# Performance work log

Measured on AMD Instinct MI355X. Metric: run time of the kernel, lower is better.

The kernel has to match this reference:

```python
import jax, jax.numpy as jnp
import numpy as np

N = 50000   # nodes (= batch_size = num_e)
D = 256     # d_dim = n_hidden
E = 320000  # edges (first half 'in' direction, second half 'out'/inverse)
R = 400     # relation types (incl. inverses)


def setup_inputs() -> dict:
    key = jax.random.key(0)
    ks = jax.random.split(key, 12)
    s = 0.05  # weight scale so tanh stays in linear-ish range
    w = lambda k, shp: jax.random.normal(k, shp, jnp.float32) * s
    return {
        "emb": jax.random.normal(ks[0], (N, D), jnp.float32),
        "edge_index": jax.random.randint(ks[1], (2, E), 0, N),
        "edge_type": jax.random.randint(ks[2], (E,), 0, R),
        "rel1": w(ks[3], (R, D)),
        "W_in1": w(ks[4], (D, D)),
        "W_out1": w(ks[5], (D, D)),
        "W_loop1": w(ks[6], (D, D)),
        "b1": jnp.zeros((D,), jnp.float32),
        "rel2": w(ks[7], (R, D)),
        "W_in2": w(ks[8], (D, D)),
        "W_out2": w(ks[9], (D, D)),
        "W_loop2": w(ks[10], (D, D)),
        "b2": jnp.zeros((D,), jnp.float32),
        "res": jnp.array([0.1], jnp.float32),
        "mu_w": w(ks[11], (D, D)),
        "mu_b": jnp.zeros((D,), jnp.float32),
        "num_nodes": N,
    }


def _mgcn_conv(x, edge_index, edge_type, rel, W_in, W_out, W_loop, b, n):
    """Relational conv: gather -> compose with relation emb -> direction-split
    linear transform -> degree-normalized scatter-add -> self-loop -> tanh."""
    src, dst = edge_index[0], edge_index[1]
    e = edge_index.shape[1]
    half = e // 2
    m = x[src] * rel[edge_type]                                   # [E, D] compose ('mult')
    m = jnp.concatenate([m[:half] @ W_in, m[half:] @ W_out], 0)    # direction-specific transform
    deg = jax.ops.segment_sum(jnp.ones((e,), x.dtype), dst, num_segments=n)
    norm = 1.0 / jnp.maximum(deg, 1.0)                             # 1/in-degree
    agg = jax.ops.segment_sum(m * norm[dst][:, None], dst, num_segments=n)
    return jnp.tanh(agg + x @ W_loop + b)


def reference(emb, edge_index, edge_type,
              rel1, W_in1, W_out1, W_loop1, b1,
              rel2, W_in2, W_out2, W_loop2, b2,
              res, mu_w, mu_b, num_nodes):
    # forward_base with p.res=True, core_layer=2, dropout in eval mode (identity)
    h = emb + res * _mgcn_conv(emb, edge_index, edge_type, rel1, W_in1, W_out1, W_loop1, b1, num_nodes)
    h = h + res * _mgcn_conv(h, edge_index, edge_type, rel2, W_in2, W_out2, W_loop2, b2, num_nodes)
    # drift head f(t, y) = mu(forward_base(y))
    return h @ mu_w + mu_b
```

## Files before the change

### kernel.cpp

```cpp
#include <hip/hip_runtime.h>
#include <hip/hip_bf16.h>
#include <cstdint>
#include <cstddef>


typedef short bf16x8 __attribute__((ext_vector_type(8)));
typedef float f32x4  __attribute__((ext_vector_type(4)));

__device__ __forceinline__ float b2f(unsigned short u) {
    union { unsigned u32; float f; } c; c.u32 = ((unsigned)u) << 16; return c.f;
}
__device__ __forceinline__ unsigned short f2b(float f) {
    union { float f; unsigned u; } c; c.f = f;
    unsigned r = c.u + 0x7FFFu + ((c.u >> 16) & 1u);
    return (unsigned short)(r >> 16);
}
__device__ __forceinline__ float ftanh(float x) {
    float e = __expf(2.0f * x);
    return 1.0f - __fdividef(2.0f, e + 1.0f);
}


__global__ void k_hist(const int* __restrict__ dst, int* __restrict__ cnt, int E) {
    int i = blockIdx.x * blockDim.x + threadIdx.x;
    if (i < E) atomicAdd(&cnt[dst[i]], 1);
}

__global__ void k_norm(const int* __restrict__ cnt, float* __restrict__ norm, int N) {
    int i = blockIdx.x * blockDim.x + threadIdx.x;
    if (i < N) norm[i] = 1.0f / fmaxf((float)cnt[i], 1.0f);
}

__global__ void k_scan1(const int* __restrict__ cnt, int* __restrict__ part,
                        int* __restrict__ bsum, int N) {
    __shared__ int s[256];
    int i = blockIdx.x * 256 + threadIdx.x;
    int v = (i < N) ? cnt[i] : 0;
    s[threadIdx.x] = v; __syncthreads();
    #pragma unroll
    for (int o = 1; o < 256; o <<= 1) {
        int t = (threadIdx.x >= o) ? s[threadIdx.x - o] : 0;
        __syncthreads();
        s[threadIdx.x] += t;
        __syncthreads();
    }
    if (i < N) part[i] = s[threadIdx.x] - v;
    if (threadIdx.x == 255) bsum[blockIdx.x] = s[255];
}

__global__ void k_scan2(int* __restrict__ bsum, int nb) {
    __shared__ int s[256];
    int v = (threadIdx.x < nb) ? bsum[threadIdx.x] : 0;
    s[threadIdx.x] = v; __syncthreads();
    #pragma unroll
    for (int o = 1; o < 256; o <<= 1) {
        int t = (threadIdx.x >= o) ? s[threadIdx.x - o] : 0;
        __syncthreads();
        s[threadIdx.x] += t;
        __syncthreads();
    }
    if (threadIdx.x < nb) bsum[threadIdx.x] = s[threadIdx.x] - v;
}

__global__ void k_scan3(const int* __restrict__ part, const int* __restrict__ bsum,
                        int* __restrict__ rowptr, int* __restrict__ cursor, int N, int E) {
    int i = blockIdx.x * 256 + threadIdx.x;
    if (i < N) {
        int r = part[i] + bsum[blockIdx.x];
        rowptr[i] = r; cursor[i] = r;
    }
    if (i == 0) rowptr[N] = E;
}

__global__ void k_scatter(const int* __restrict__ src, const int* __restrict__ dst,
                          const int* __restrict__ et, int* __restrict__ cursor,
                          unsigned* __restrict__ erec, int E, int halfE) {
    int e = blockIdx.x * blockDim.x + threadIdx.x;
    if (e < E) {
        int d = dst[e];
        int pos = atomicAdd(&cursor[d], 1);
        unsigned rec = (unsigned)src[e] | ((unsigned)et[e] << 16)
                     | ((e >= halfE) ? 0x80000000u : 0u);
        erec[pos] = rec;
    }
}


__global__ void k_cvt3(const float* __restrict__ s0, unsigned short* __restrict__ d0, long n0,
                       const float* __restrict__ s1, unsigned short* __restrict__ d1, long n1,
                       const float* __restrict__ s2, unsigned short* __restrict__ d2, long n2) {
    long i = (long)blockIdx.x * blockDim.x + threadIdx.x;
    const float* s; unsigned short* d; long j = i;
    if (j < n0) { s = s0; d = d0; }
    else {
        j -= n0;
        if (j < n1) { s = s1; d = d1; }
        else { j -= n1; if (j >= n2) return; s = s2; d = d2; }
    }
    float4 v = ((const float4*)s)[j];
    ushort4 o;
    o.x = f2b(v.x); o.y = f2b(v.y); o.z = f2b(v.z); o.w = f2b(v.w);
    ((ushort4*)d)[j] = o;
}

__global__ void k_wfrag7(const float* __restrict__ w0, const float* __restrict__ w1,
                         const float* __restrict__ w2, const float* __restrict__ w3,
                         const float* __restrict__ w4, const float* __restrict__ w5,
                         const float* __restrict__ w6, unsigned short* __restrict__ out) {
    int o = blockIdx.x * 256 + threadIdx.x;
    int mi = o >> 16;
    int r  = o & 65535;
    const float* W = (mi == 0) ? w0 : (mi == 1) ? w1 : (mi == 2) ? w2 :
                     (mi == 3) ? w3 : (mi == 4) ? w4 : (mi == 5) ? w5 : w6;
    int j  = r & 7;
    int l  = (r >> 3) & 63;
    int nn = (r >> 9) & 15;
    int kg = r >> 13;
    int k = kg * 32 + (l >> 4) * 8 + j;
    int n = nn * 16 + (l & 15);
    out[o] = f2b(W[k * 256 + n]);
}


__global__ __launch_bounds__(256)
void k_agg(const unsigned short* __restrict__ xb, const unsigned short* __restrict__ relb,
           const int* __restrict__ rowptr, const unsigned* __restrict__ erec,
           const float* __restrict__ norm,
           unsigned short* __restrict__ sIn, unsigned short* __restrict__ sOut,
           int N, int D)
{
    const int w = threadIdx.x >> 6, l = threadIdx.x & 63;
    const int v = blockIdx.x * 4 + w;
    if (v >= N) return;
    const int rs = rowptr[v], re = rowptr[v + 1];
    const float nm = norm[v];

    float ai0 = 0, ai1 = 0, ai2 = 0, ai3 = 0;
    float ao0 = 0, ao1 = 0, ao2 = 0, ao3 = 0;

    unsigned c0 = (rs     < re) ? erec[rs]     : 0u;
    unsigned c1 = (rs + 1 < re) ? erec[rs + 1] : 0u;
    unsigned c2 = (rs + 2 < re) ? erec[rs + 2] : 0u;
    unsigned c3 = (rs + 3 < re) ? erec[rs + 3] : 0u;
    int i = rs;
    while (i + 4 <= re) {
        unsigned m0 = (i + 4 < re) ? erec[i + 4] : 0u;
        unsigned m1 = (i + 5 < re) ? erec[i + 5] : 0u;
        unsigned m2 = (i + 6 < re) ? erec[i + 6] : 0u;
        unsigned m3 = (i + 7 < re) ? erec[i + 7] : 0u;
        ushort4 x0 = *(const ushort4*)(xb   + (size_t)(c0 & 0xffff) * D + l * 4);
        ushort4 r0 = *(const ushort4*)(relb + (size_t)((c0 >> 16) & 0x7fff) * D + l * 4);
        ushort4 x1 = *(const ushort4*)(xb   + (size_t)(c1 & 0xffff) * D + l * 4);
        ushort4 r1 = *(const ushort4*)(relb + (size_t)((c1 >> 16) & 0x7fff) * D + l * 4);
        ushort4 x2 = *(const ushort4*)(xb   + (size_t)(c2 & 0xffff) * D + l * 4);
        ushort4 r2 = *(const ushort4*)(relb + (size_t)((c2 >> 16) & 0x7fff) * D + l * 4);
        ushort4 x3 = *(const ushort4*)(xb   + (size_t)(c3 & 0xffff) * D + l * 4);
        ushort4 r3 = *(const ushort4*)(relb + (size_t)((c3 >> 16) & 0x7fff) * D + l * 4);
        float p0, p1, p2, p3;
        p0 = b2f(x0.x)*b2f(r0.x); p1 = b2f(x0.y)*b2f(r0.y);
        p2 = b2f(x0.z)*b2f(r0.z); p3 = b2f(x0.w)*b2f(r0.w);
        if (c0 >> 31) { ao0 += p0; ao1 += p1; ao2 += p2; ao3 += p3; }
        else          { ai0 += p0; ai1 += p1; ai2 += p2; ai3 += p3; }
        p0 = b2f(x1.x)*b2f(r1.x); p1 = b2f(x1.y)*b2f(r1.y);
        p2 = b2f(x1.z)*b2f(r1.z); p3 = b2f(x1.w)*b2f(r1.w);
        if (c1 >> 31) { ao0 += p0; ao1 += p1; ao2 += p2; ao3 += p3; }
        else          { ai0 += p0; ai1 += p1; ai2 += p2; ai3 += p3; }
        p0 = b2f(x2.x)*b2f(r2.x); p1 = b2f(x2.y)*b2f(r2.y);
        p2 = b2f(x2.z)*b2f(r2.z); p3 = b2f(x2.w)*b2f(r2.w);
        if (c2 >> 31) { ao0 += p0; ao1 += p1; ao2 += p2; ao3 += p3; }
        else          { ai0 += p0; ai1 += p1; ai2 += p2; ai3 += p3; }
        p0 = b2f(x3.x)*b2f(r3.x); p1 = b2f(x3.y)*b2f(r3.y);
        p2 = b2f(x3.z)*b2f(r3.z); p3 = b2f(x3.w)*b2f(r3.w);
        if (c3 >> 31) { ao0 += p0; ao1 += p1; ao2 += p2; ao3 += p3; }
        else          { ai0 += p0; ai1 += p1; ai2 += p2; ai3 += p3; }
        c0 = m0; c1 = m1; c2 = m2; c3 = m3; i += 4;
    }
    #pragma unroll
    for (int j = 0; j < 3; ++j) {
        if (i + j < re) {
            unsigned cur = (j == 0) ? c0 : (j == 1) ? c1 : c2;
            ushort4 x0 = *(const ushort4*)(xb   + (size_t)(cur & 0xffff) * D + l * 4);
            ushort4 r0 = *(const ushort4*)(relb + (size_t)((cur >> 16) & 0x7fff) * D + l * 4);
            float p0 = b2f(x0.x)*b2f(r0.x), p1 = b2f(x0.y)*b2f(r0.y);
            float p2 = b2f(x0.z)*b2f(r0.z), p3 = b2f(x0.w)*b2f(r0.w);
            if (cur >> 31) { ao0 += p0; ao1 += p1; ao2 += p2; ao3 += p3; }
            else           { ai0 += p0; ai1 += p1; ai2 += p2; ai3 += p3; }
        }
    }

    ushort4 oi, oo;
    oi.x = f2b(ai0 * nm); oi.y = f2b(ai1 * nm); oi.z = f2b(ai2 * nm); oi.w = f2b(ai3 * nm);
    oo.x = f2b(ao0 * nm); oo.y = f2b(ao1 * nm); oo.z = f2b(ao2 * nm); oo.w = f2b(ao3 * nm);
    *(ushort4*)(sIn  + (size_t)v * D + l * 4) = oi;
    *(ushort4*)(sOut + (size_t)v * D + l * 4) = oo;
}


__global__ __launch_bounds__(256, 2)
void k_gemmW(const unsigned short* __restrict__ a0,
             const unsigned short* __restrict__ a1,
             const unsigned short* __restrict__ a2,
             const unsigned short* __restrict__ Wf,
             const float* __restrict__ bias,
             const float* __restrict__ resPtr,
             unsigned short* __restrict__ outB,
             int N, int D)
{
    __shared__ unsigned short lds[4][2][4096];

    const int t = threadIdx.x;
    const int rBase = blockIdx.x * 64;
    const int w  = t >> 6;
    const int l  = t & 63;
    const int lr = l & 15;
    const int lq = l >> 4;

    size_t gRow[8];
    #pragma unroll
    for (int j = 0; j < 8; ++j)
        gRow[j] = (size_t)min(rBase + j * 8 + (l >> 3), N - 1) * 256 + (l & 7) * 8;
    const int woBase = (l >> 3) * 64 + (((l & 7) ^ (l >> 3)) * 8);

    f32x4 acc[4][4] = {};
    uint4 Rg[8];

    #pragma unroll
    for (int j = 0; j < 8; ++j)
        Rg[j] = *(const uint4*)(a0 + gRow[j]);
    #pragma unroll
    for (int j = 0; j < 8; ++j)
        *(uint4*)(&lds[w][0][woBase + j * 512]) = Rg[j];
    #pragma unroll
    for (int j = 0; j < 8; ++j)
        Rg[j] = *(const uint4*)(a0 + gRow[j] + 64);

    #pragma unroll
    for (int s = 0; s < 12; ++s) {
        const unsigned short* __restrict__ At = lds[w][s & 1];
        const int p = s >> 2, cb = s & 3;
        const unsigned short* __restrict__ Wp = Wf + (size_t)p * 65536;

        if (s + 1 < 12) {
            unsigned short* An = &lds[w][(s + 1) & 1][0];
            #pragma unroll
            for (int j = 0; j < 8; ++j)
                *(uint4*)(&An[woBase + j * 512]) = Rg[j];
        }
        if (s + 2 < 12) {
            const int p2 = (s + 2) >> 2, cb2 = (s + 2) & 3;
            const unsigned short* ap = (p2 == 0) ? a0 : ((p2 == 1) ? a1 : a2);
            #pragma unroll
            for (int j = 0; j < 8; ++j)
                Rg[j] = *(const uint4*)(ap + gRow[j] + cb2 * 64);
        }
        (void)cb;

        #pragma unroll
        for (int kk = 0; kk < 2; ++kk) {
            const int kg = cb * 2 + kk;
            bf16x8 a_[4], b_[4];
            #pragma unroll
            for (int m = 0; m < 4; ++m) {
                int rm = 16 * m + lr;
                int ch = (kk * 4 + lq) ^ (rm & 7);
                a_[m] = *(const bf16x8*)(&At[rm * 64 + ch * 8]);
            }
            #pragma unroll
            for (int n = 0; n < 4; ++n)
                b_[n] = *(const bf16x8*)(Wp + (((kg * 16 + (w * 4 + n)) * 64 + l) * 8));
            #pragma unroll
            for (int m = 0; m < 4; ++m) {
                #pragma unroll
                for (int n = 0; n < 4; ++n)
                    acc[m][n] = __builtin_amdgcn_mfma_f32_16x16x32_bf16(a_[m], b_[n], acc[m][n], 0, 0, 0);
            }
        }
    }

    const int rb4 = lq * 4;
    const float resv = resPtr[0];
    unsigned short* C = (unsigned short*)lds;
    __syncthreads();
    #pragma unroll
    for (int half = 0; half < 2; ++half) {
        if (half) __syncthreads();
        if ((w >> 1) == half) {
            #pragma unroll
            for (int m = 0; m < 4; ++m) {
                #pragma unroll
                for (int i = 0; i < 4; ++i) {
                    int r6 = 16 * m + rb4 + i;
                    #pragma unroll
                    for (int n = 0; n < 4; ++n) {
                        int cH = (w & 1) * 64 + lr + 16 * n;
                        float v = acc[m][n][i] + bias[half * 128 + cH];
                        C[r6 * 128 + cH] = f2b(resv * ftanh(v));
                    }
                }
            }
        }
        __syncthreads();
        #pragma unroll
        for (int ii = 0; ii < 4; ++ii) {
            int g   = ii * 256 + t;
            int r   = g >> 4;
            int cc  = g & 15;
            int row = rBase + r;
            if (row < N) {
                bf16x8 sv = *(const bf16x8*)(&C[r * 128 + cc * 8]);
                const unsigned short* ar = a0 + (size_t)row * D + half * 128 + cc * 8;
                uint4 av = *(const uint4*)ar;
                unsigned aw[4] = { av.x, av.y, av.z, av.w };
                unsigned ow[4];
                #pragma unroll
                for (int p = 0; p < 4; ++p) {
                    float h0 = b2f((unsigned short)(aw[p] & 0xffff)) + b2f((unsigned short)sv[2 * p]);
                    float h1 = b2f((unsigned short)(aw[p] >> 16))    + b2f((unsigned short)sv[2 * p + 1]);
                    ow[p] = (unsigned)f2b(h0) | ((unsigned)f2b(h1) << 16);
                }
                *(uint4*)(outB + (size_t)row * D + half * 128 + cc * 8) =
                    make_uint4(ow[0], ow[1], ow[2], ow[3]);
            }
        }
    }
}


#define GIT(S, AtC, AtN, Rw0, Rw1, Rl0, Rl1, Bc, Bn)                            \
  do {                                                                          \
    if ((S) + 1 < 12) {                                                         \
      *(uint4*)(&AtN[wo0]) = Rw0;                                               \
      *(uint4*)(&AtN[wo1]) = Rw1;                                               \
    }                                                                           \
    if ((S) + 1 < 12) {                                                         \
      const int pn_ = ((S) + 1) >> 2, cbn_ = ((S) + 1) & 3;                     \
      const unsigned short* __restrict__ Wn_ = Wf + (size_t)pn_ * 65536;        \
      _Pragma("unroll")                                                         \
      for (int kk_ = 0; kk_ < 2; ++kk_) {                                       \
        _Pragma("unroll")                                                       \
        for (int n_ = 0; n_ < 4; ++n_) {                                        \
          Bn[kk_ * 4 + n_] = *(const bf16x8*)(Wn_ +                             \
              ((((cbn_ * 2 + kk_) * 16 + (w * 4 + n_)) * 64 + l) * 8));         \
        }                                                                       \
      }                                                                         \
    }                                                                           \
    {                                                                           \
      const int cb_ = (S) & 3;                                                  \
      _Pragma("unroll")                                                         \
      for (int kk_ = 0; kk_ < 2; ++kk_) {                                       \
        (void)cb_;                                                              \
        bf16x8 a_[4];                                                           \
        _Pragma("unroll")                                                       \
        for (int m_ = 0; m_ < 4; ++m_) {                                        \
          int rm_ = 16 * m_ + lr;                                               \
          int ch_ = (kk_ * 4 + lq) ^ (rm_ & 7);                                 \
          a_[m_] = *(const bf16x8*)(&AtC[rm_ * 64 + ch_ * 8]);                  \
        }                                                                       \
        _Pragma("unroll")                                                       \
        for (int m_ = 0; m_ < 4; ++m_) {                                        \
          _Pragma("unroll")                                                     \
          for (int n_ = 0; n_ < 4; ++n_) {                                      \
            acc[m_][n_] = __builtin_amdgcn_mfma_f32_16x16x32_bf16(a_[m_], Bc[kk_ * 4 + n_], acc[m_][n_], 0, 0, 0); \
          }                                                                     \
        }                                                                       \
      }                                                                         \
    }                                                                           \
    if ((S) + 3 < 12) {                                                         \
      const int p3_ = ((S) + 3) >> 2, cb3_ = ((S) + 3) & 3;                     \
      const unsigned short* ap_ = (p3_ == 0) ? a0 : ((p3_ == 1) ? a1 : a2);     \
      Rl0 = *(const uint4*)(ap_ + g0 + cb3_ * 64);                              \
      Rl1 = *(const uint4*)(ap_ + g1 + cb3_ * 64);                              \
    }                                                                           \
    asm volatile("s_waitcnt lgkmcnt(0)" ::: "memory");                          \
    __builtin_amdgcn_sched_barrier(0);                                          \
    __builtin_amdgcn_s_barrier();                                               \
    __builtin_amdgcn_sched_barrier(0);                                          \
  } while (0)

template <bool HEAD>
__global__ __launch_bounds__(256, 2)
void k_gemm(const unsigned short* __restrict__ a0,
            const unsigned short* __restrict__ a1,
            const unsigned short* __restrict__ a2,
            const unsigned short* __restrict__ Wf,
            const float* __restrict__ bias,
            const float* __restrict__ resPtr,
            const unsigned short* __restrict__ WfMu,
            const float* __restrict__ mub,
            float* __restrict__ outF,
            unsigned short* __restrict__ outB,
            int N, int D)
{
    __shared__ unsigned short lds[HEAD ? 16384 : 8192];
    unsigned short* At0 = lds;
    unsigned short* At1 = lds + 4096;

    const int t = threadIdx.x;
    const int rBase = blockIdx.x * 64;

    const int w  = t >> 6;
    const int l  = t & 63;
    const int lr = l & 15;
    const int lq = l >> 4;

    const int rS0 = t >> 3;
    const int rS1 = rS0 + 32;
    const int cS  = t & 7;
    const int wo0 = rS0 * 64 + ((cS ^ (rS0 & 7)) * 8);
    const int wo1 = rS1 * 64 + ((cS ^ (rS1 & 7)) * 8);
    const size_t g0 = (size_t)min(rBase + rS0, N - 1) * D + cS * 8;
    const size_t g1 = (size_t)min(rBase + rS1, N - 1) * D + cS * 8;

    f32x4 acc[4][4] = {};
    uint4 Ra0, Ra1, Rb0, Rb1, Rc0, Rc1;
    bf16x8 B0[8], B1[8];

    Ra0 = *(const uint4*)(a0 + g0);
    Ra1 = *(const uint4*)(a0 + g1);
    Rb0 = *(const uint4*)(a0 + g0 + 64);
    Rb1 = *(const uint4*)(a0 + g1 + 64);
    Rc0 = *(const uint4*)(a0 + g0 + 128);
    Rc1 = *(const uint4*)(a0 + g1 + 128);
    #pragma unroll
    for (int kk = 0; kk < 2; ++kk) {
        #pragma unroll
        for (int n = 0; n < 4; ++n)
            B0[kk * 4 + n] = *(const bf16x8*)(Wf + (((kk * 16 + (w * 4 + n)) * 64 + l) * 8));
    }
    *(uint4*)(&At0[wo0]) = Ra0;
    *(uint4*)(&At0[wo1]) = Ra1;
    asm volatile("s_waitcnt lgkmcnt(0)" ::: "memory");
    __builtin_amdgcn_sched_barrier(0);
    __builtin_amdgcn_s_barrier();
    __builtin_amdgcn_sched_barrier(0);

    GIT(0,  At0, At1, Rb0, Rb1, Ra0, Ra1, B0, B1);
    GIT(1,  At1, At0, Rc0, Rc1, Rb0, Rb1, B1, B0);
    GIT(2,  At0, At1, Ra0, Ra1, Rc0, Rc1, B0, B1);
    GIT(3,  At1, At0, Rb0, Rb1, Ra0, Ra1, B1, B0);
    GIT(4,  At0, At1, Rc0, Rc1, Rb0, Rb1, B0, B1);
    GIT(5,  At1, At0, Ra0, Ra1, Rc0, Rc1, B1, B0);
    GIT(6,  At0, At1, Rb0, Rb1, Ra0, Ra1, B0, B1);
    GIT(7,  At1, At0, Rc0, Rc1, Rb0, Rb1, B1, B0);
    GIT(8,  At0, At1, Ra0, Ra1, Rc0, Rc1, B0, B1);
    GIT(9,  At1, At0, Rb0, Rb1, Ra0, Ra1, B1, B0);
    GIT(10, At0, At1, Rc0, Rc1, Rb0, Rb1, B0, B1);
    GIT(11, At1, At0, Ra0, Ra1, Rc0, Rc1, B1, B0);

    const int rb4 = lq * 4;
    const float resv = resPtr[0];

    if (!HEAD) {
        unsigned short* C = lds;
        #pragma unroll
        for (int half = 0; half < 2; ++half) {
            if ((w >> 1) == half) {
                #pragma unroll
                for (int m = 0; m < 4; ++m) {
                    #pragma unroll
                    for (int i = 0; i < 4; ++i) {
                        int r6 = 16 * m + rb4 + i;
                        #pragma unroll
                        for (int n = 0; n < 4; ++n) {
                            int cH = (w & 1) * 64 + lr + 16 * n;
                            float v = acc[m][n][i] + bias[half * 128 + cH];
                            C[r6 * 128 + cH] = f2b(resv * ftanh(v));
                        }
                    }
                }
            }
            __syncthreads();
            #pragma unroll
            for (int ii = 0; ii < 4; ++ii) {
                int g   = ii * 256 + t;
                int r   = g >> 4;
                int cc  = g & 15;
                int row = rBase + r;
                if (row < N) {
                    bf16x8 sv = *(const bf16x8*)(&C[r * 128 + cc * 8]);
                    const unsigned short* ar = a0 + (size_t)row * D + half * 128 + cc * 8;
                    uint4 av = *(const uint4*)ar;
                    unsigned aw[4] = { av.x, av.y, av.z, av.w };
                    unsigned ow[4];
                    #pragma unroll
                    for (int p = 0; p < 4; ++p) {
                        float h0 = b2f((unsigned short)(aw[p] & 0xffff)) + b2f((unsigned short)sv[2 * p]);
                        float h1 = b2f((unsigned short)(aw[p] >> 16))    + b2f((unsigned short)sv[2 * p + 1]);
                        ow[p] = (unsigned)f2b(h0) | ((unsigned)f2b(h1) << 16);
                    }
                    *(uint4*)(outB + (size_t)row * D + half * 128 + cc * 8) =
                        make_uint4(ow[0], ow[1], ow[2], ow[3]);
                }
            }
            __syncthreads();
        }
    } else {
        #pragma unroll
        for (int m = 0; m < 4; ++m) {
            #pragma unroll
            for (int i = 0; i < 4; ++i) {
                int row = rBase + 16 * m + rb4 + i;
                if (row < N) {
                    size_t base = (size_t)row * D + w * 64 + lr;
                    int r6 = 16 * m + rb4 + i;
                    #pragma unroll
                    for (int n = 0; n < 4; ++n) {
                        int   c = w * 64 + lr + 16 * n;
                        float v = acc[m][n][i] + bias[c];
                        float h = b2f(a0[base + 16 * n]) + resv * ftanh(v);
                        lds[r6 * 256 + (c ^ ((r6 & 7) << 3))] = f2b(h);
                    }
                }
            }
        }
        __syncthreads();
        #pragma unroll
        for (int m = 0; m < 4; ++m) {
            #pragma unroll
            for (int n = 0; n < 4; ++n)
                acc[m][n] = (f32x4){0.f, 0.f, 0.f, 0.f};
        }

        #pragma unroll
        for (int s2 = 0; s2 < 4; ++s2) {
            #pragma unroll
            for (int kk = 0; kk < 2; ++kk) {
                const int kg = s2 * 2 + kk;
                bf16x8 a_[4], b_[4];
                #pragma unroll
                for (int m = 0; m < 4; ++m) {
                    int rm = 16 * m + lr;
                    int ch = (s2 * 8 + kk * 4 + lq) ^ (rm & 7);
                    a_[m] = *(const bf16x8*)(&lds[rm * 256 + ch * 8]);
                }
                #pragma unroll
                for (int n = 0; n < 4; ++n)
                    b_[n] = *(const bf16x8*)(WfMu + (((kg * 16 + (w * 4 + n)) * 64 + l) * 8));
                #pragma unroll
                for (int m = 0; m < 4; ++m) {
                    #pragma unroll
                    for (int n = 0; n < 4; ++n)
                        acc[m][n] = __builtin_amdgcn_mfma_f32_16x16x32_bf16(a_[m], b_[n], acc[m][n], 0, 0, 0);
                }
            }
        }

        __syncthreads();
        float* Cf = (float*)lds;
        #pragma unroll
        for (int half = 0; half < 2; ++half) {
            if ((w >> 1) == half) {
                #pragma unroll
                for (int m = 0; m < 4; ++m) {
                    #pragma unroll
                    for (int i = 0; i < 4; ++i) {
                        int r6 = 16 * m + rb4 + i;
                        #pragma unroll
                        for (int n = 0; n < 4; ++n) {
                            int cH = (w & 1) * 64 + lr + 16 * n;
                            Cf[r6 * 128 + cH] = acc[m][n][i] + mub[half * 128 + cH];
                        }
                    }
                }
            }
            __syncthreads();
            #pragma unroll
            for (int ii = 0; ii < 8; ++ii) {
                int g   = ii * 256 + t;
                int r   = g >> 5;
                int cc  = g & 31;
                int row = rBase + r;
                if (row < N) {
                    *(float4*)(outF + (size_t)row * D + half * 128 + cc * 4) =
                        *(const float4*)(&Cf[r * 128 + cc * 4]);
                }
            }
            __syncthreads();
        }
    }
}


extern "C" void kernel_launch(void* const* d_in, const int* in_sizes, int n_in,
                              void* d_out, int out_size, void* d_ws, size_t ws_size,
                              hipStream_t stream)
{
    const float* emb  = (const float*)d_in[0];
    const int*   ei   = (const int*)  d_in[1];
    const int*   et   = (const int*)  d_in[2];
    const float* rel1 = (const float*)d_in[3];
    const float* Wi1  = (const float*)d_in[4];
    const float* Wo1  = (const float*)d_in[5];
    const float* Wl1  = (const float*)d_in[6];
    const float* b1   = (const float*)d_in[7];
    const float* rel2 = (const float*)d_in[8];
    const float* Wi2  = (const float*)d_in[9];
    const float* Wo2  = (const float*)d_in[10];
    const float* Wl2  = (const float*)d_in[11];
    const float* b2   = (const float*)d_in[12];
    const float* res  = (const float*)d_in[13];
    const float* muw  = (const float*)d_in[14];
    const float* mub  = (const float*)d_in[15];

    const int D = in_sizes[7];
    const int N = in_sizes[0] / D;
    const int E = in_sizes[2];
    const int R = in_sizes[3] / D;
    const int halfE = E / 2;
    const int* srcA = ei;
    const int* dstA = ei + E;
    const size_t DD = (size_t)D * D;

    char* ws = (char*)d_ws;
    size_t off = 0;
    auto alloc = [&](size_t bytes) -> char* {
        char* p = ws + off; off += (bytes + 255) & ~(size_t)255; return p;
    };
    const int nb1 = (N + 255) / 256;

    float*          norm   = (float*)          alloc((size_t)N * 4);
    int*            cnt    = (int*)            alloc((size_t)N * 4);
    int*            rowptr = (int*)            alloc((size_t)(N + 1) * 4);
    int*            cursor = (int*)            alloc((size_t)N * 4);
    int*            part   = (int*)            alloc((size_t)N * 4);
    int*            bsum   = (int*)            alloc(1024);
    unsigned*       erec   = (unsigned*)       alloc((size_t)E * 4);
    unsigned short* xb     = (unsigned short*) alloc((size_t)N * D * 2);
    unsigned short* h1b    = (unsigned short*) alloc((size_t)N * D * 2);
    unsigned short* sIn    = (unsigned short*) alloc((size_t)N * D * 2);
    unsigned short* sOut   = (unsigned short*) alloc((size_t)N * D * 2);
    unsigned short* r1b    = (unsigned short*) alloc((size_t)R * D * 2);
    unsigned short* r2b    = (unsigned short*) alloc((size_t)R * D * 2);
    unsigned short* fAll   = (unsigned short*) alloc(7 * DD * 2);
    if (off > ws_size) return;

    unsigned short* fW1 = fAll;
    unsigned short* fW2 = fAll + 3 * DD;
    unsigned short* fMu = fAll + 6 * DD;

    hipMemsetAsync(cnt, 0, (size_t)N * 4, stream);
    k_hist   <<<(E + 255) / 256, 256, 0, stream>>>(dstA, cnt, E);
    k_norm   <<<nb1, 256, 0, stream>>>(cnt, norm, N);
    k_scan1  <<<nb1, 256, 0, stream>>>(cnt, part, bsum, N);
    k_scan2  <<<1,   256, 0, stream>>>(bsum, nb1);
    k_scan3  <<<nb1, 256, 0, stream>>>(part, bsum, rowptr, cursor, N, E);
    k_scatter<<<(E + 255) / 256, 256, 0, stream>>>(srcA, dstA, et, cursor, erec, E, halfE);

    long nd4 = (long)N * D / 4, rd4 = (long)R * D / 4;
    long tot4 = nd4 + 2 * rd4;
    k_cvt3<<<(int)((tot4 + 255) / 256), 256, 0, stream>>>(
        emb, xb, nd4, rel1, r1b, rd4, rel2, r2b, rd4);
    k_wfrag7<<<(int)(7 * DD / 256), 256, 0, stream>>>(
        Wl1, Wi1, Wo1, Wl2, Wi2, Wo2, muw, fAll);

    const int AB = (N + 3) / 4;
    const int NB = (N + 63) / 64;

    k_agg<<<AB, 256, 0, stream>>>(xb, r1b, rowptr, erec, norm, sIn, sOut, N, D);
    k_gemmW<<<NB, 256, 0, stream>>>(xb, sIn, sOut, fW1, b1, res, h1b, N, D);

    k_agg<<<AB, 256, 0, stream>>>(h1b, r2b, rowptr, erec, norm, sIn, sOut, N, D);
    k_gemm<true><<<NB, 256, 0, stream>>>(h1b, sIn, sOut, fW2, b2, res,
                                         fMu, mub, (float*)d_out, nullptr, N, D);
}
```

Measured before the change: 239.3 us.

## Use half-wave edge split in layer-1 aggregation and 512-thread shared-tile GEMM

Adds k_agg2, in which each half of a wavefront handles alternate edges with 16-byte loads covering all 256 columns, and the two halves' partial sums are combined with a cross-half shuffle. It also replaces the layer-1 GEMM with a 512-thread kernel where all eight waves share one 64-row A tile in LDS, with triple-register prefetch and block barriers between steps. The goals are more memory-level parallelism in the gather and less per-wave LDS use with higher occupancy in the GEMM. The cost is extra barriers and a shuffle reduction, and only layer 1 uses the new kernels.

```diff
diff --git a/kernel.cpp b/kernel.cpp
--- a/kernel.cpp
+++ b/kernel.cpp
@@ -119,6 +119,95 @@
     int k = kg * 32 + (l >> 4) * 8 + j;
     int n = nn * 16 + (l & 15);
     out[o] = f2b(W[k * 256 + n]);
+}
+
+
+__global__ __launch_bounds__(256)
+void k_agg2(const unsigned short* __restrict__ xb, const unsigned short* __restrict__ relb,
+            const int* __restrict__ rowptr, const unsigned* __restrict__ erec,
+            const float* __restrict__ norm,
+            unsigned short* __restrict__ sIn, unsigned short* __restrict__ sOut,
+            int N, int D)
+{
+    const int w = threadIdx.x >> 6, l = threadIdx.x & 63;
+    const int v = blockIdx.x * 4 + w;
+    if (v >= N) return;
+    const int rs = rowptr[v], re = rowptr[v + 1];
+    const float nm = norm[v];
+    const int h  = l >> 5;
+    const int sl = l & 31;
+
+    float ai[8] = {}, ao[8] = {};
+
+    #pragma unroll 1
+    for (int i = rs; i < re; i += 4) {
+        const int e0 = i + h, e1 = i + 2 + h;
+        const unsigned c0 = (e0 < re) ? erec[e0] : 0u;
+        const unsigned c1 = (e1 < re) ? erec[e1] : 0u;
+        uint4 x0 = make_uint4(0,0,0,0), r0 = make_uint4(0,0,0,0);
+        uint4 x1 = make_uint4(0,0,0,0), r1 = make_uint4(0,0,0,0);
+        if (e0 < re) {
+            x0 = *(const uint4*)(xb   + (size_t)(c0 & 0xffff) * 256 + sl * 8);
+            r0 = *(const uint4*)(relb + (size_t)((c0 >> 16) & 0x7fff) * 256 + sl * 8);
+        }
+        if (e1 < re) {
+            x1 = *(const uint4*)(xb   + (size_t)(c1 & 0xffff) * 256 + sl * 8);
+            r1 = *(const uint4*)(relb + (size_t)((c1 >> 16) & 0x7fff) * 256 + sl * 8);
+        }
+        {
+            unsigned xs[4] = { x0.x, x0.y, x0.z, x0.w };
+            unsigned rv[4] = { r0.x, r0.y, r0.z, r0.w };
+            if (c0 >> 31) {
+                #pragma unroll
+                for (int p = 0; p < 4; ++p) {
+                    ao[2*p]   += b2f((unsigned short)(xs[p] & 0xffff)) * b2f((unsigned short)(rv[p] & 0xffff));
+                    ao[2*p+1] += b2f((unsigned short)(xs[p] >> 16))    * b2f((unsigned short)(rv[p] >> 16));
+                }
+            } else {
+                #pragma unroll
+                for (int p = 0; p < 4; ++p) {
+                    ai[2*p]   += b2f((unsigned short)(xs[p] & 0xffff)) * b2f((unsigned short)(rv[p] & 0xffff));
+                    ai[2*p+1] += b2f((unsigned short)(xs[p] >> 16))    * b2f((unsigned short)(rv[p] >> 16));
+                }
+            }
+        }
+        {
+            unsigned xs[4] = { x1.x, x1.y, x1.z, x1.w };
+            unsigned rv[4] = { r1.x, r1.y, r1.z, r1.w };
+            if (c1 >> 31) {
+                #pragma unroll
+                for (int p = 0; p < 4; ++p) {
+                    ao[2*p]   += b2f((unsigned short)(xs[p] & 0xffff)) * b2f((unsigned short)(rv[p] & 0xffff));
+                    ao[2*p+1] += b2f((unsigned short)(xs[p] >> 16))    * b2f((unsigned short)(rv[p] >> 16));
+                }
+            } else {
+                #pragma unroll
+                for (int p = 0; p < 4; ++p) {
+                    ai[2*p]   += b2f((unsigned short)(xs[p] & 0xffff)) * b2f((unsigned short)(rv[p] & 0xffff));
+                    ai[2*p+1] += b2f((unsigned short)(xs[p] >> 16))    * b2f((unsigned short)(rv[p] >> 16));
+                }
+            }
+        }
+    }
+
+    #pragma unroll
+    for (int j = 0; j < 8; ++j) {
+        ai[j] += __shfl_xor(ai[j], 32, 64);
+        ao[j] += __shfl_xor(ao[j], 32, 64);
+    }
+
+    unsigned ow[4];
+    if (h == 0) {
+        #pragma unroll
+        for (int p = 0; p < 4; ++p)
+            ow[p] = (unsigned)f2b(ai[2*p] * nm) | ((unsigned)f2b(ai[2*p+1] * nm) << 16);
+        *(uint4*)(sIn + (size_t)v * 256 + sl * 8) = make_uint4(ow[0], ow[1], ow[2], ow[3]);
+    } else {
+        #pragma unroll
+        for (int p = 0; p < 4; ++p)
+            ow[p] = (unsigned)f2b(ao[2*p] * nm) | ((unsigned)f2b(ao[2*p+1] * nm) << 16);
+        *(uint4*)(sOut + (size_t)v * 256 + sl * 8) = make_uint4(ow[0], ow[1], ow[2], ow[3]);
+    }
 }
 
 
@@ -196,103 +285,115 @@
 }
 
 
-__global__ __launch_bounds__(256, 2)
-void k_gemmW(const unsigned short* __restrict__ a0,
-             const unsigned short* __restrict__ a1,
-             const unsigned short* __restrict__ a2,
-             const unsigned short* __restrict__ Wf,
-             const float* __restrict__ bias,
-             const float* __restrict__ resPtr,
-             unsigned short* __restrict__ outB,
-             int N, int D)
+#define GIT512(S, AtC, AtN, Rw, Rl)                                            \
+  do {                                                                         \
+    if ((S) + 1 < 12) {                                                        \
+      *(uint4*)(&AtN[wo]) = Rw;                                                \
+    }                                                                          \
+    {                                                                          \
+      const int p_ = (S) >> 2, cb_ = (S) & 3;                                  \
+      const unsigned short* __restrict__ Wp_ = Wf + (size_t)p_ * 65536;        \
+      _Pragma("unroll")                                                        \
+      for (int kk_ = 0; kk_ < 2; ++kk_) {                                      \
+        const int kg_ = cb_ * 2 + kk_;                                         \
+        bf16x8 a_[2], b_[4];                                                   \
+        _Pragma("unroll")                                                      \
+        for (int m_ = 0; m_ < 2; ++m_) {                                       \
+          int rm_ = 32 * wm + 16 * m_ + lr;                                    \
+          int ch_ = (kk_ * 4 + lq) ^ (rm_ & 7);                                \
+          a_[m_] = *(const bf16x8*)(&AtC[rm_ * 64 + ch_ * 8]);                 \
+        }                                                                      \
+        _Pragma("unroll")                                                      \
+        for (int n_ = 0; n_ < 4; ++n_) {                                       \
+          b_[n_] = *(const bf16x8*)(Wp_ + (((kg_ * 16 + (wcol * 4 + n_)) * 64 + l) * 8)); \
+        }                                                                      \
+        _Pragma("unroll")                                                      \
+        for (int m_ = 0; m_ < 2; ++m_) {                                       \
+          _Pragma("unroll")                                                    \
+          for (int n_ = 0; n_ < 4; ++n_) {                                     \
+            acc[m_][n_] = __builtin_amdgcn_mfma_f32_16x16x32_bf16(a_[m_], b_[n_], acc[m_][n_], 0, 0, 0); \
+          }                                                                    \
+        }                                                                      \
+      }                                                                        \
+    }                                                                          \
+    if ((S) + 3 < 12) {                                                        \
+      const int p3_ = ((S) + 3) >> 2, cb3_ = ((S) + 3) & 3;                    \
+      const unsigned short* ap_ = (p3_ == 0) ? a0 : ((p3_ == 1) ? a1 : a2);    \
+      Rl = *(const uint4*)(ap_ + g + cb3_ * 64);                               \
+    }                                                                          \
+    asm volatile("s_waitcnt lgkmcnt(0)" ::: "memory");                         \
+    __builtin_amdgcn_sched_barrier(0);                                         \
+    __builtin_amdgcn_s_barrier();                                              \
+    __builtin_amdgcn_sched_barrier(0);                                         \
+  } while (0)
+
+__global__ __launch_bounds__(512, 6)
+void k_gemm512(const unsigned short* __restrict__ a0,
+               const unsigned short* __restrict__ a1,
+               const unsigned short* __restrict__ a2,
+               const unsigned short* __restrict__ Wf,
+               const float* __restrict__ bias,
+               const float* __restrict__ resPtr,
+               unsigned short* __restrict__ outB,
+               int N, int D)
 {
-    __shared__ unsigned short lds[4][2][4096];
+    __shared__ unsigned short lds[8192];
+    unsigned short* At0 = lds;
+    unsigned short* At1 = lds + 4096;
 
     const int t = threadIdx.x;
     const int rBase = blockIdx.x * 64;
-    const int w  = t >> 6;
+    const int w    = t >> 6;
+    const int wcol = w & 3;
+    const int wm   = w >> 2;
     const int l  = t & 63;
     const int lr = l & 15;
     const int lq = l >> 4;
 
-    size_t gRow[8];
-    #pragma unroll
-    for (int j = 0; j < 8; ++j)
-        gRow[j] = (size_t)min(rBase + j * 8 + (l >> 3), N - 1) * 256 + (l & 7) * 8;
-    const int woBase = (l >> 3) * 64 + (((l & 7) ^ (l >> 3)) * 8);
-
-    f32x4 acc[4][4] = {};
-    uint4 Rg[8];
-
-    #pragma unroll
-    for (int j = 0; j < 8; ++j)
-        Rg[j] = *(const uint4*)(a0 + gRow[j]);
-    #pragma unroll
-    for (int j = 0; j < 8; ++j)
-        *(uint4*)(&lds[w][0][woBase + j * 512]) = Rg[j];
-    #pragma unroll
-    for (int j = 0; j < 8; ++j)
-        Rg[j] = *(const uint4*)(a0 + gRow[j] + 64);
-
-    #pragma unroll
-    for (int s = 0; s < 12; ++s) {
-        const unsigned short* __restrict__ At = lds[w][s & 1];
-        const int p = s >> 2, cb = s & 3;
-        const unsigned short* __restrict__ Wp = Wf + (size_t)p * 65536;
-
-        if (s + 1 < 12) {
-            unsigned short* An = &lds[w][(s + 1) & 1][0];
-            #pragma unroll
-            for (int j = 0; j < 8; ++j)
-                *(uint4*)(&An[woBase + j * 512]) = Rg[j];
-        }
-        if (s + 2 < 12) {
-            const int p2 = (s + 2) >> 2, cb2 = (s + 2) & 3;
-            const unsigned short* ap = (p2 == 0) ? a0 : ((p2 == 1) ? a1 : a2);
-            #pragma unroll
-            for (int j = 0; j < 8; ++j)
-                Rg[j] = *(const uint4*)(ap + gRow[j] + cb2 * 64);
-        }
-        (void)cb;
-
-        #pragma unroll
-        for (int kk = 0; kk < 2; ++kk) {
-            const int kg = cb * 2 + kk;
-            bf16x8 a_[4], b_[4];
-            #pragma unroll
-            for (int m = 0; m < 4; ++m) {
-                int rm = 16 * m + lr;
-                int ch = (kk * 4 + lq) ^ (rm & 7);
-                a_[m] = *(const bf16x8*)(&At[rm * 64 + ch * 8]);
-            }
-            #pragma unroll
-            for (int n = 0; n < 4; ++n)
-                b_[n] = *(const bf16x8*)(Wp + (((kg * 16 + (w * 4 + n)) * 64 + l) * 8));
-            #pragma unroll
-            for (int m = 0; m < 4; ++m) {
-                #pragma unroll
-                for (int n = 0; n < 4; ++n)
-                    acc[m][n] = __builtin_amdgcn_mfma_f32_16x16x32_bf16(a_[m], b_[n], acc[m][n], 0, 0, 0);
-            }
-        }
-    }
+    const int rS = t >> 3;
+    const int cS = t & 7;
+    const int wo = rS * 64 + ((cS ^ (rS & 7)) * 8);
+    const size_t g = (size_t)min(rBase + rS, N - 1) * 256 + cS * 8;
+
+    f32x4 acc[2][4] = {};
+    uint4 Ra, Rb, Rc;
+
+    Ra = *(const uint4*)(a0 + g);
+    Rb = *(const uint4*)(a0 + g + 64);
+    Rc = *(const uint4*)(a0 + g + 128);
+    *(uint4*)(&At0[wo]) = Ra;
+    asm volatile("s_waitcnt lgkmcnt(0)" ::: "memory");
+    __builtin_amdgcn_sched_barrier(0);
+    __builtin_amdgcn_s_barrier();
+    __builtin_amdgcn_sched_barrier(0);
+
+    GIT512(0,  At0, At1, Rb, Ra);
+    GIT512(1,  At1, At0, Rc, Rb);
+    GIT512(2,  At0, At1, Ra, Rc);
+    GIT512(3,  At1, At0, Rb, Ra);
+    GIT512(4,  At0, At1, Rc, Rb);
+    GIT512(5,  At1, At0, Ra, Rc);
+    GIT512(6,  At0, At1, Rb, Ra);
+    GIT512(7,  At1, At0, Rc, Rb);
+    GIT512(8,  At0, At1, Ra, Rc);
+    GIT512(9,  At1, At0, Rb, Ra);
+    GIT512(10, At0, At1, Rc, Rb);
+    GIT512(11, At1, At0, Ra, Rc);
 
     const int rb4 = lq * 4;
     const float resv = resPtr[0];
-    unsigned short* C = (unsigned short*)lds;
-    __syncthreads();
+    unsigned short* C = lds;
     #pragma unroll
     for (int half = 0; half < 2; ++half) {
-        if (half) __syncthreads();
-        if ((w >> 1) == half) {
+        if ((wcol >> 1) == half) {
             #pragma unroll
-            for (int m = 0; m < 4; ++m) {
+            for (int m = 0; m < 2; ++m) {
                 #pragma unroll
                 for (int i = 0; i < 4; ++i) {
-                    int r6 = 16 * m + rb4 + i;
+                    int r6 = 32 * wm + 16 * m + rb4 + i;
                     #pragma unroll
                     for (int n = 0; n < 4; ++n) {
-                        int cH = (w & 1) * 64 + lr + 16 * n;
+                        int cH = (wcol & 1) * 64 + lr + 16 * n;
                         float v = acc[m][n][i] + bias[half * 128 + cH];
                         C[r6 * 128 + cH] = f2b(resv * ftanh(v));
                     }
@@ -301,10 +402,10 @@
         }
         __syncthreads();
         #pragma unroll
-        for (int ii = 0; ii < 4; ++ii) {
-            int g   = ii * 256 + t;
-            int r   = g >> 4;
-            int cc  = g & 15;
+        for (int ii = 0; ii < 2; ++ii) {
+            int g2  = ii * 512 + t;
+            int r   = g2 >> 4;
+            int cc  = g2 & 15;
             int row = rBase + r;
             if (row < N) {
                 bf16x8 sv = *(const bf16x8*)(&C[r * 128 + cc * 8]);
@@ -322,6 +423,7 @@
                     make_uint4(ow[0], ow[1], ow[2], ow[3]);
             }
         }
+        __syncthreads();
     }
 }
 
@@ -656,8 +758,8 @@
     const int AB = (N + 3) / 4;
     const int NB = (N + 63) / 64;
 
-    k_agg<<<AB, 256, 0, stream>>>(xb, r1b, rowptr, erec, norm, sIn, sOut, N, D);
-    k_gemmW<<<NB, 256, 0, stream>>>(xb, sIn, sOut, fW1, b1, res, h1b, N, D);
+    k_agg2<<<AB, 256, 0, stream>>>(xb, r1b, rowptr, erec, norm, sIn, sOut, N, D);
+    k_gemm512<<<NB, 512, 0, stream>>>(xb, sIn, sOut, fW1, b1, res, h1b, N, D);
 
     k_agg<<<AB, 256, 0, stream>>>(h1b, r2b, rowptr, erec, norm, sIn, sOut, N, D);
     k_gemm<true><<<NB, 256, 0, stream>>>(h1b, sIn, sOut, fW2, b2, res,
```

New measurement: 245.7 us. +2.7%, slower.
